# Performance work log

Hardware: AMD Instinct MI355X
Metric: run time of the kernel (lower is better)

The kernel has to match this reference:

```python
import jax, jax.numpy as jnp
import numpy as np
from jax import lax

N, C, H, W = 32, 128, 64, 64
EPS = 1e-5


def conv2d(x, w, stride=1, pad=0, dil=1, groups=1):
    return lax.conv_general_dilated(
        x, w, (stride, stride), [(pad, pad), (pad, pad)],
        rhs_dilation=(dil, dil), feature_group_count=groups,
        dimension_numbers=('NCHW', 'OIHW', 'NCHW'))


def bn(y):  # BatchNorm2d(affine=False), training-mode batch stats
    m = y.mean((0, 2, 3), keepdims=True)
    v = y.var((0, 2, 3), keepdims=True)
    return (y - m) * lax.rsqrt(v + EPS)


def max_pool3(x):
    return lax.reduce_window(x, -jnp.inf, lax.max, (1, 1, 3, 3), (1, 1, 1, 1),
                             [(0, 0), (0, 0), (1, 1), (1, 1)])


def avg_pool3(x):  # count_include_pad=False
    s = lax.reduce_window(x, 0., lax.add, (1, 1, 3, 3), (1, 1, 1, 1),
                          [(0, 0), (0, 0), (1, 1), (1, 1)])
    ones = jnp.ones((1, 1, x.shape[2], x.shape[3]), x.dtype)
    cnt = lax.reduce_window(ones, 0., lax.add, (1, 1, 3, 3), (1, 1, 1, 1),
                            [(0, 0), (0, 0), (1, 1), (1, 1)])
    return s / cnt


def setup_inputs() -> dict:
    key = jax.random.key(0)
    ks = jax.random.split(key, 20)
    sc = 0.05
    inp = {
        'x': jax.random.normal(ks[0], (N, C, H, W), jnp.float32),
        'weights': jax.random.uniform(ks[1], (8,), jnp.float32),
        'ca_fc1': jax.random.normal(ks[2], (C // 2, C, 1, 1), jnp.float32) * sc,
        'ca_fc2': jax.random.normal(ks[3], (C, C // 2, 1, 1), jnp.float32) * sc,
        'sa_conv': jax.random.normal(ks[4], (1, 2, 7, 7), jnp.float32) * sc,
        'sep3_dw1': jax.random.normal(ks[5], (C, 1, 3, 3), jnp.float32) * sc,
        'sep3_pw1': jax.random.normal(ks[6], (C, C, 1, 1), jnp.float32) * sc,
        'sep3_dw2': jax.random.normal(ks[7], (C, 1, 3, 3), jnp.float32) * sc,
        'sep3_pw2': jax.random.normal(ks[8], (C, C, 1, 1), jnp.float32) * sc,
        'sep5_dw1': jax.random.normal(ks[9], (C, 1, 5, 5), jnp.float32) * sc,
        'sep5_pw1': jax.random.normal(ks[10], (C, C, 1, 1), jnp.float32) * sc,
        'sep5_dw2': jax.random.normal(ks[11], (C, 1, 5, 5), jnp.float32) * sc,
        'sep5_pw2': jax.random.normal(ks[12], (C, C, 1, 1), jnp.float32) * sc,
        'dil3_dw': jax.random.normal(ks[13], (C, 1, 3, 3), jnp.float32) * sc,
        'dil3_pw': jax.random.normal(ks[14], (C, C, 1, 1), jnp.float32) * sc,
        'dil5_dw': jax.random.normal(ks[15], (C, 1, 5, 5), jnp.float32) * sc,
        'dil5_pw': jax.random.normal(ks[16], (C, C, 1, 1), jnp.float32) * sc,
        # stand-in for the random distinct bottom-quarter index selection
        'perm_idx': jax.random.permutation(ks[17], C // 4).astype(jnp.int32),
    }
    return inp


def _forward(x, weights, ca_fc1, ca_fc2, sa_conv,
             sep3_dw1, sep3_pw1, sep3_dw2, sep3_pw2,
             sep5_dw1, sep5_pw1, sep5_dw2, sep5_pw2,
             dil3_dw, dil3_pw, dil5_dw, dil5_pw, perm_idx):
    c = x.shape[1]
    # ---- spatial attention ----
    s = jnp.concatenate([x.mean(1, keepdims=True), x.max(1, keepdims=True)], 1)
    x = x * jax.nn.sigmoid(conv2d(s, sa_conv, pad=3))
    # ---- channel attention ----
    mlp = lambda z: conv2d(jax.nn.relu(conv2d(z, ca_fc1)), ca_fc2)
    att = jax.nn.sigmoid(mlp(x.mean((2, 3), keepdims=True)) +
                         mlp(x.max((2, 3), keepdims=True)))  # [N,C,1,1]
    x = x * att
    # ---- channel selection: top 3/4 by summed attention + permuted quarter ----
    slist = att.sum(0).reshape(c)
    _, top_idx = lax.top_k(slist, c * 3 // 4)
    num_dict = jnp.concatenate([top_idx.astype(jnp.int32), perm_idx])  # [C]
    xt = x[:, num_dict]
    # ---- 8 DARTS candidate ops, weighted sum ----
    def sep(y, dw1, pw1, dw2, pw2, pad):
        y = jax.nn.relu(y)
        y = bn(conv2d(conv2d(y, dw1, pad=pad, groups=c), pw1))
        y = jax.nn.relu(y)
        return bn(conv2d(conv2d(y, dw2, pad=pad, groups=c), pw2))

    def dil(y, dw, pw, pad):
        y = jax.nn.relu(y)
        return bn(conv2d(conv2d(y, dw, pad=pad, dil=2, groups=c), pw))

    temp1 = (weights[0] * jnp.zeros_like(xt)            # none
             + weights[1] * bn(max_pool3(xt))            # max_pool_3x3 + BN
             + weights[2] * bn(avg_pool3(xt))            # avg_pool_3x3 + BN
             + weights[3] * xt                           # skip_connect (stride=1)
             + weights[4] * sep(xt, sep3_dw1, sep3_pw1, sep3_dw2, sep3_pw2, 1)
             + weights[5] * sep(xt, sep5_dw1, sep5_pw1, sep5_dw2, sep5_pw2, 2)
             + weights[6] * dil(xt, dil3_dw, dil3_pw, 2)
             + weights[7] * dil(xt, dil5_dw, dil5_pw, 4))
    # scatter back (stride=1 => spatial sizes match)
    return x.at[:, num_dict].set(temp1)


def reference(x, weights, ca_fc1, ca_fc2, sa_conv,
              sep3_dw1, sep3_pw1, sep3_dw2, sep3_pw2,
              sep5_dw1, sep5_pw1, sep5_dw2, sep5_pw2,
              dil3_dw, dil3_pw, dil5_dw, dil5_pw, perm_idx):
    return _forward(x, weights, ca_fc1, ca_fc2, sa_conv,
                    sep3_dw1, sep3_pw1, sep3_dw2, sep3_pw2,
                    sep5_dw1, sep5_pw1, sep5_dw2, sep5_pw2,
                    dil3_dw, dil3_pw, dil5_dw, dil5_pw, perm_idx)
```

## Files before the change

kernel.cpp:

```cpp
#include <hip/hip_runtime.h>
#include <math.h>

#define DI __device__ __forceinline__
typedef unsigned short ush;

DI float u2f(ush u){ return __uint_as_float(((unsigned int)u)<<16); }
DI ush f2u(float f){ unsigned int u=__float_as_uint(f); u += 0x7fffu + ((u>>16)&1u); return (ush)(u>>16); }

constexpr int HWc = 4096;
constexpr float RCNT = 1.f/131072.f;
constexpr size_t BIG = 33554432ull;

typedef __attribute__((ext_vector_type(8))) __bf16 bf8;
typedef __attribute__((ext_vector_type(4))) float  f4;

DI void unp8(uint4 q, float* o){
  o[0]=u2f((ush)(q.x&0xffff)); o[1]=u2f((ush)(q.x>>16));
  o[2]=u2f((ush)(q.y&0xffff)); o[3]=u2f((ush)(q.y>>16));
  o[4]=u2f((ush)(q.z&0xffff)); o[5]=u2f((ush)(q.z>>16));
  o[6]=u2f((ush)(q.w&0xffff)); o[7]=u2f((ush)(q.w>>16));
}
DI uint4 pk8(const ush* u){
  uint4 q;
  q.x=(unsigned)u[0]|((unsigned)u[1]<<16); q.y=(unsigned)u[2]|((unsigned)u[3]<<16);
  q.z=(unsigned)u[4]|((unsigned)u[5]<<16); q.w=(unsigned)u[6]|((unsigned)u[7]<<16);
  return q;
}

__global__ void k_zero2(float* __restrict__ a, float* __restrict__ b){
  int i=blockIdx.x*256+threadIdx.x;
  if(i<2048) a[i]=0.f;
  else if(i<2048+49152) b[i-2048]=0.f;
}

__global__ void k_trivial(float* __restrict__ out){
  size_t i=(size_t)blockIdx.x*256+threadIdx.x;
  if(i<16777216ull) out[i]=0.f;
}

__global__ void k_chan_reduce(const float* __restrict__ x, float* __restrict__ smean, float* __restrict__ smax){
  int n = blockIdx.y;
  int px = blockIdx.x*256 + threadIdx.x;
  const float* xp = x + ((size_t)n*128)*HWc + px;
  float s=0.f, m=-INFINITY;
  #pragma unroll 8
  for(int c=0;c<128;c++){ float v=xp[(size_t)c*HWc]; s+=v; m=fmaxf(m,v); }
  smean[n*HWc+px]=s*(1.f/128.f);
  smax[n*HWc+px]=m;
}

__global__ void k_sa(const float* __restrict__ smean, const float* __restrict__ smax,
                     const float* __restrict__ w, float* __restrict__ sa){
  __shared__ float wm[49], wx[49];
  int t=threadIdx.x;
  if(t<49) wm[t]=w[t];
  else if(t<98) wx[t-49]=w[t];
  __syncthreads();
  int n=blockIdx.y;
  int px=blockIdx.x*256+t;
  int r=px>>6, c=px&63;
  const float* pm  = smean + n*HWc;
  const float* pxm = smax  + n*HWc;
  float acc=0.f;
  for(int ky=0;ky<7;ky++){
    int rr=r+ky-3; if(rr<0||rr>=64) continue;
    for(int kx=0;kx<7;kx++){
      int cc=c+kx-3; if(cc<0||cc>=64) continue;
      int q=(rr<<6)+cc;
      acc += wm[ky*7+kx]*pm[q] + wx[ky*7+kx]*pxm[q];
    }
  }
  sa[n*HWc+px] = 1.f/(1.f+expf(-acc));
}

__global__ void k_rowred(const float* __restrict__ x, const float* __restrict__ sa,
                         float* __restrict__ rsum, float* __restrict__ rmax){
  int c=blockIdx.x, n=blockIdx.y;
  const float* xp = x + ((size_t)n*128 + c)*HWc;
  const float* sp = sa + n*HWc;
  float s=0.f, m=-INFINITY;
  for(int i=threadIdx.x;i<HWc;i+=256){
    float v=xp[i]*sp[i]; s+=v; m=fmaxf(m,v);
  }
  __shared__ float ls[4], lm[4];
  for(int o=32;o>0;o>>=1){ s+=__shfl_down(s,o,64); m=fmaxf(m,__shfl_down(m,o,64)); }
  int lane=threadIdx.x&63, wv=threadIdx.x>>6;
  if(lane==0){ ls[wv]=s; lm[wv]=m; }
  __syncthreads();
  if(threadIdx.x==0){
    rsum[n*128+c]=ls[0]+ls[1]+ls[2]+ls[3];
    rmax[n*128+c]=fmaxf(fmaxf(lm[0],lm[1]),fmaxf(lm[2],lm[3]));
  }
}

__global__ void k_mlp(const float* __restrict__ rsum, const float* __restrict__ rmax,
                      const float* __restrict__ fc1, const float* __restrict__ fc2,
                      float* __restrict__ att){
  int n=blockIdx.x, t=threadIdx.x;
  __shared__ float zm[128], zx[128], hm[64], hx[64];
  if(t<128){ zm[t]=rsum[n*128+t]*(1.f/4096.f); zx[t]=rmax[n*128+t]; }
  __syncthreads();
  if(t<64){
    float a=0.f;
    for(int c=0;c<128;c++) a+=fc1[t*128+c]*zm[c];
    hm[t]=fmaxf(a,0.f);
  } else if(t<128){
    int j=t-64; float a=0.f;
    for(int c=0;c<128;c++) a+=fc1[j*128+c]*zx[c];
    hx[j]=fmaxf(a,0.f);
  }
  __syncthreads();
  if(t<128){
    float a=0.f,b=0.f;
    for(int j=0;j<64;j++){ float wv=fc2[t*64+j]; a+=wv*hm[j]; b+=wv*hx[j]; }
    att[n*128+t]=1.f/(1.f+expf(-(a+b)));
  }
}

__global__ void k_topk(const float* __restrict__ att, const int* __restrict__ perm,
                       int* __restrict__ nd_out, int* __restrict__ dst_pos){
  __shared__ float sl[128];
  __shared__ int nd[128];
  int t=threadIdx.x;
  float s=0.f;
  for(int n=0;n<32;n++) s+=att[n*128+t];
  sl[t]=s;
  nd[t]=t;
  __syncthreads();
  float v=sl[t]; int r=0;
  for(int c=0;c<128;c++){ float u=sl[c]; r += ((u>v) || (u==v && c<t)) ? 1 : 0; }
  if(r<96) nd[r]=t;
  __syncthreads();
  if(t<32) nd[96+t]=perm[t]&127;
  __syncthreads();
  nd_out[t]=nd[t]&127;
  int pos=-1;
  for(int p=0;p<128;p++) if((nd[p]&127)==t) pos=p;
  dst_pos[t]=pos;
}

template<int R,int S>
DI void stage_pads(float* __restrict__ Pl, int t){
  if(t<64){
    #pragma unroll
    for(int j=0;j<R;j++) Pl[t*S+j]=0.f;
    #pragma unroll
    for(int j=64+R;j<S;j++) Pl[t*S+j]=0.f;
  }
}

__global__ void k_cvt6(const float* __restrict__ a,const float* __restrict__ b,
    const float* __restrict__ c,const float* __restrict__ d,
    const float* __restrict__ e,const float* __restrict__ f,
    ush* __restrict__ wb){
  int z=blockIdx.y;
  const float* src = z==0?a:z==1?b:z==2?c:z==3?d:z==4?e:f;
  int i=blockIdx.x*256+threadIdx.x;
  wb[z*16384+i]=f2u(src[i]);
}

__global__ __launch_bounds__(256) void k_xtps(const float* __restrict__ x,
    const float* __restrict__ sa, const float* __restrict__ att,
    const int* __restrict__ nd, ush* __restrict__ bufX, float* __restrict__ stats){
  constexpr int S=68;
  __shared__ float Pl[64*S];
  int p=blockIdx.x, n=blockIdx.y, t=threadIdx.x;
  int ch=nd[p]&127;
  float a=att[n*128+ch];
  const float* xp=x+((size_t)n*128+ch)*HWc;
  const float* sp=sa+n*HWc;
  int px0=t*16;
  ush u[16];
  #pragma unroll
  for(int j=0;j<4;j++){
    float4 xv=*(const float4*)(xp+px0+4*j);
    float4 sv=*(const float4*)(sp+px0+4*j);
    u[4*j+0]=f2u(xv.x*sv.x*a); u[4*j+1]=f2u(xv.y*sv.y*a);
    u[4*j+2]=f2u(xv.z*sv.z*a); u[4*j+3]=f2u(xv.w*sv.w*a);
  }
  ush* bo=bufX+((size_t)n*128+p)*HWc+px0;
  *(uint4*)bo   = pk8(u);
  *(uint4*)(bo+8)= pk8(u+8);
  float* dst=&Pl[(px0>>6)*S + 1 + (px0&63)];
  #pragma unroll
  for(int i=0;i<16;i++) dst[i]=u2f(u[i]);
  stage_pads<1,S>(Pl,t);
  __syncthreads();
  int r=t>>2, c0=(t&3)*16;
  float s[16], m[16];
  #pragma unroll
  for(int i=0;i<16;i++){ s[i]=0.f; m[i]=-INFINITY; }
  int rin=0;
  #pragma unroll
  for(int ky=-1;ky<=1;ky++){
    int rr=r+ky;
    if(rr<0||rr>=64) continue;
    rin++;
    float row[20];
    #pragma unroll
    for(int j=0;j<5;j++) *(float4*)&row[4*j] = *(const float4*)&Pl[rr*S + c0 + 4*j];
    float e0  = (c0==0)  ? -INFINITY : row[0];
    float e17 = (c0==48) ? -INFINITY : row[17];
    #pragma unroll
    for(int i=0;i<16;i++){
      float lf = (i==0)  ? e0  : row[i];
      float rg = (i==15) ? e17 : row[i+2];
      s[i] += row[i]+row[i+1]+row[i+2];
      m[i] = fmaxf(m[i], fmaxf(lf, fmaxf(row[i+1], rg)));
    }
  }
  float sm=0,qm=0,sv=0,qv=0;
  #pragma unroll
  for(int i=0;i<16;i++){
    int c=c0+i;
    float cnt=(float)(rin*(3-(c==0)-(c==63)));
    float ap=s[i]/cnt, mp=m[i];
    sm+=mp; qm+=mp*mp; sv+=ap; qv+=ap*ap;
  }
  for(int o=32;o>0;o>>=1){
    sm+=__shfl_down(sm,o,64); qm+=__shfl_down(qm,o,64);
    sv+=__shfl_down(sv,o,64); qv+=__shfl_down(qv,o,64);
  }
  __shared__ float l[4][4];
  int lane=t&63, wv=t>>6;
  if(lane==0){ l[wv][0]=sm; l[wv][1]=qm; l[wv][2]=sv; l[wv][3]=qv; }
  __syncthreads();
  if(t==0){
    atomicAdd(&stats[p],     l[0][0]+l[1][0]+l[2][0]+l[3][0]);
    atomicAdd(&stats[128+p], l[0][1]+l[1][1]+l[2][1]+l[3][1]);
    atomicAdd(&stats[256+p], l[0][2]+l[1][2]+l[2][2]+l[3][2]);
    atomicAdd(&stats[384+p], l[0][3]+l[1][3]+l[2][3]+l[3][3]);
  }
}

template<int KS,int DIL,int BN>
DI void dw_core(float* Pl, const ush* src, const float* __restrict__ dww,
                const float* __restrict__ fin, int p,int n,int t, ush* outb){
  constexpr int R=(KS/2)*DIL;
  constexpr int S=(R==4)?76:68;
  constexpr int NL=(16+2*R+3)/4;
  float mean=0.f, rstd=0.f;
  if constexpr(BN){ mean=fin[p]; rstd=fin[128+p]; }
  const ush* bp = src + ((size_t)n*128+p)*HWc;
  int px0=t*16;
  uint4 va=*(const uint4*)(bp+px0);
  uint4 vb=*(const uint4*)(bp+px0+8);
  float* dst=&Pl[(px0>>6)*S + R + (px0&63)];
  unsigned int wv8[8]={va.x,va.y,va.z,va.w,vb.x,vb.y,vb.z,vb.w};
  #pragma unroll
  for(int j=0;j<8;j++){
    float v0=u2f((ush)(wv8[j]&0xffff)), v1=u2f((ush)(wv8[j]>>16));
    if constexpr(BN){ v0=(v0-mean)*rstd; v1=(v1-mean)*rstd; }
    dst[2*j]  =fmaxf(v0,0.f);
    dst[2*j+1]=fmaxf(v1,0.f);
  }
  stage_pads<R,S>(Pl,t);
  __syncthreads();
  float wk[KS*KS];
  #pragma unroll
  for(int i=0;i<KS*KS;i++) wk[i]=dww[p*KS*KS+i];
  int r=t>>2, c0=(t&3)*16;
  float acc[16];
  #pragma unroll
  for(int i=0;i<16;i++) acc[i]=0.f;
  #pragma unroll
  for(int ky=0;ky<KS;ky++){
    int rr=r+(ky-KS/2)*DIL;
    if(rr<0||rr>=64) continue;
    float row[NL*4];
    #pragma unroll
    for(int j=0;j<NL;j++) *(float4*)&row[4*j] = *(const float4*)&Pl[rr*S + c0 + 4*j];
    #pragma unroll
    for(int kx=0;kx<KS;kx++){
      float wv=wk[ky*KS+kx];
      #pragma unroll
      for(int i=0;i<16;i++) acc[i]+=wv*row[R + i + (kx-KS/2)*DIL];
    }
  }
  ush* op = outb + ((size_t)n*128+p)*HWc + r*64 + c0;
  #pragma unroll
  for(int q=0;q<4;q++){
    ushort4 vv;
    vv.x=f2u(acc[4*q+0]); vv.y=f2u(acc[4*q+1]);
    vv.z=f2u(acc[4*q+2]); vv.w=f2u(acc[4*q+3]);
    *(ushort4*)(op+4*q)=vv;
  }
}

__global__ __launch_bounds__(256) void k_dw4(const ush* __restrict__ bufX,
    const float* __restrict__ s3d1,const float* __restrict__ s5d1,
    const float* __restrict__ d3dw,const float* __restrict__ d5dw,
    ush* __restrict__ bufA, ush* __restrict__ bufB,
    ush* __restrict__ bufC, ush* __restrict__ bufD){
  __shared__ float Pl[64*76];
  int p=blockIdx.x,n=blockIdx.y,t=threadIdx.x,z=blockIdx.z;
  if(z==0)      dw_core<3,1,0>(Pl,bufX,s3d1,nullptr,p,n,t,bufA);
  else if(z==1) dw_core<5,1,0>(Pl,bufX,s5d1,nullptr,p,n,t,bufB);
  else if(z==2) dw_core<3,2,0>(Pl,bufX,d3dw,nullptr,p,n,t,bufC);
  else          dw_core<5,2,0>(Pl,bufX,d5dw,nullptr,p,n,t,bufD);
}

__global__ __launch_bounds__(256) void k_dw2(ush* bufA, ush* bufB,
    const float* __restrict__ s3d2,const float* __restrict__ s5d2,
    const float* __restrict__ fin0,const float* __restrict__ fin2){
  __shared__ float Pl[64*68];
  int p=blockIdx.x,n=blockIdx.y,t=threadIdx.x,z=blockIdx.z;
  if(z==0) dw_core<3,1,1>(Pl,bufA,s3d2,fin0,p,n,t,bufA);
  else     dw_core<5,1,1>(Pl,bufB,s5d2,fin2,p,n,t,bufB);
}

DI void pw_core(char* pool, const ush* dwin, const ush* __restrict__ wt,
                ush* outb, float* __restrict__ shad, int bx,int by,int t){
  ush (*Bt)[132] = (ush(*)[132])pool;
  float* Lf = (float*)pool;
  int n=by;
  int px0b = bx*64;
  const ush* dp = dwin + ((size_t)n*128)*HWc + px0b;
  #pragma unroll
  for(int k=0;k<4;k++){
    int e = t + k*256;
    int c2 = e>>4;
    int p4 = (e&15)*4;
    const ush* g0 = dp + (size_t)(2*c2)*HWc + p4;
    ushort4 va = *(const ushort4*)g0;
    ushort4 vb = *(const ushort4*)(g0 + HWc);
    *(unsigned int*)&Bt[p4+0][2*c2] = (unsigned int)va.x | ((unsigned int)vb.x<<16);
    *(unsigned int*)&Bt[p4+1][2*c2] = (unsigned int)va.y | ((unsigned int)vb.y<<16);
    *(unsigned int*)&Bt[p4+2][2*c2] = (unsigned int)va.z | ((unsigned int)vb.z<<16);
    *(unsigned int*)&Bt[p4+3][2*c2] = (unsigned int)va.w | ((unsigned int)vb.w<<16);
  }
  int lane=t&63, wv=t>>6;
  int co0=(wv>>1)*64, pxw=(wv&1)*32;
  int g=lane>>4, sl=lane&15;
  int arow = co0 + sl;
  int acg  = g*8;
  bf8 a[4][4];
  #pragma unroll
  for(int mt=0;mt<4;mt++)
    #pragma unroll
    for(int kt=0;kt<4;kt++)
      a[mt][kt] = *(const bf8*)(wt + (size_t)(arow+mt*16)*128 + kt*32 + acg);
  f4 acc[4][2] = {};
  __syncthreads();
  #pragma unroll
  for(int nt=0;nt<2;nt++){
    int pxl = pxw + nt*16 + sl;
    bf8 b[4];
    #pragma unroll
    for(int kt=0;kt<4;kt++){
      union { uint2 h[2]; bf8 v; } u;
      const ush* bp = &Bt[pxl][kt*32 + acg];
      u.h[0] = *(const uint2*)bp;
      u.h[1] = *(const uint2*)(bp+4);
      b[kt] = u.v;
    }
    #pragma unroll
    for(int kt=0;kt<4;kt++)
      #pragma unroll
      for(int mt=0;mt<4;mt++)
        acc[mt][nt] = __builtin_amdgcn_mfma_f32_16x16x32_bf16(a[mt][kt], b[kt], acc[mt][nt], 0,0,0);
  }
  __syncthreads();
  #pragma unroll
  for(int mt=0;mt<4;mt++)
    #pragma unroll
    for(int r=0;r<4;r++){
      int co = co0 + mt*16 + g*4 + r;
      Lf[co*66 + pxw + sl]      = acc[mt][0][r];
      Lf[co*66 + pxw + 16 + sl] = acc[mt][1][r];
    }
  __syncthreads();
  int co=t>>1, half=t&1;
  const float* Lr = &Lf[co*66 + half*32];
  float s1=0.f, s2=0.f;
  ush ob16[32];
  #pragma unroll
  for(int j=0;j<16;j++){
    float2 v=*(const float2*)(Lr+2*j);
    s1+=v.x+v.y; s2+=v.x*v.x+v.y*v.y;
    ob16[2*j]=f2u(v.x); ob16[2*j+1]=f2u(v.y);
  }
  s1+=__shfl_xor(s1,1,64); s2+=__shfl_xor(s2,1,64);
  ush* op = outb + ((size_t)n*128+co)*HWc + px0b + half*32;
  *(uint4*)op      = pk8(ob16);
  *(uint4*)(op+8)  = pk8(ob16+8);
  *(uint4*)(op+16) = pk8(ob16+16);
  *(uint4*)(op+24) = pk8(ob16+24);
  float* sh = shad + (((bx + by)&31)*256);
  if(half==0){ atomicAdd(&sh[co],s1); atomicAdd(&sh[128+co],s2); }
}

__global__ __launch_bounds__(256) void k_pw4(ush* bA, ush* bB, ush* bC, ush* bD,
    const ush* __restrict__ w0,const ush* __restrict__ w1,
    const ush* __restrict__ w2,const ush* __restrict__ w3,
    float* __restrict__ s0,float* __restrict__ s1,
    float* __restrict__ s2,float* __restrict__ s3){
  __shared__ __align__(16) char pool[33792];
  int z=blockIdx.z;
  ush* b = z==0?bA:z==1?bB:z==2?bC:bD;
  const ush* wt = z==0?w0:z==1?w1:z==2?w2:w3;
  float* sh = z==0?s0:z==1?s1:z==2?s2:s3;
  pw_core(pool,b,wt,b,sh,blockIdx.x,blockIdx.y,threadIdx.x);
}

__global__ void k_statfin4(const float* __restrict__ s0,const float* __restrict__ s1,
    const float* __restrict__ s2,const float* __restrict__ s3,
    float* __restrict__ f0,float* __restrict__ f1,
    float* __restrict__ f2,float* __restrict__ f3){
  int z=blockIdx.x, t=threadIdx.x;
  const float* shd = z==0?s0:z==1?s1:z==2?s2:s3;
  float* fin = z==0?f0:z==1?f1:z==2?f2:f3;
  if(t<128){
    float su=0.f, sq=0.f;
    #pragma unroll
    for(int j=0;j<32;j++){ su+=shd[j*256+t]; sq+=shd[j*256+128+t]; }
    float mean=su*RCNT, var=sq*RCNT-mean*mean;
    fin[t]=mean;
    fin[128+t]=rsqrtf(var+1e-5f);
  }
}

__global__ __launch_bounds__(256) void k_bacc(const float* __restrict__ x,
    const float* __restrict__ sa, const float* __restrict__ att,
    const int* __restrict__ nd, const int* __restrict__ dpos,
    const float* __restrict__ stats,
    const float* __restrict__ fin1,const float* __restrict__ fin3,
    const float* __restrict__ fin4,const float* __restrict__ fin5,
    const float* __restrict__ wts, const ush* __restrict__ bufX,
    const ush* __restrict__ brA,const ush* __restrict__ brB,
    const ush* __restrict__ brC,const ush* __restrict__ brD,
    float* __restrict__ out){
  constexpr int S=68;
  __shared__ float Pl[64*S];
  int ch=blockIdx.x, n=blockIdx.y, t=threadIdx.x;
  int p=dpos[ch];
  if(p<0){
    float a=att[n*128+ch];
    const float* xp=x+((size_t)n*128+ch)*HWc;
    const float* sp=sa+n*HWc;
    float* op=out+((size_t)n*128+ch)*HWc;
    int px0=t*16;
    #pragma unroll
    for(int j=0;j<4;j++){
      float4 xv=*(const float4*)(xp+px0+4*j);
      float4 sv=*(const float4*)(sp+px0+4*j);
      float4 ov;
      ov.x=xv.x*sv.x*a; ov.y=xv.y*sv.y*a; ov.z=xv.z*sv.z*a; ov.w=xv.w*sv.w*a;
      *(float4*)(op+px0+4*j)=ov;
    }
    return;
  }
  const ush* bxp=bufX+((size_t)n*128+p)*HWc;
  int px0=t*16;
  uint4 qa=*(const uint4*)(bxp+px0), qb=*(const uint4*)(bxp+px0+8);
  {
    float tv[16];
    unp8(qa,tv); unp8(qb,tv+8);
    float* dst=&Pl[(px0>>6)*S + 1 + (px0&63)];
    #pragma unroll
    for(int i=0;i<16;i++) dst[i]=tv[i];
  }
  stage_pads<1,S>(Pl,t);
  __syncthreads();
  float w1=wts[1],w2=wts[2],w3=wts[3],w4=wts[4],w5=wts[5],w6=wts[6],w7=wts[7];
  float m0,r0v,m1,r1v;
  { float su=stats[p],     sq=stats[128+p]; float mean=su*RCNT,var=sq*RCNT-mean*mean; m0=mean; r0v=rsqrtf(var+1e-5f); }
  { float su=stats[256+p], sq=stats[384+p]; float mean=su*RCNT,var=sq*RCNT-mean*mean; m1=mean; r1v=rsqrtf(var+1e-5f); }
  float mA=fin1[p],rA=fin1[128+p], mB=fin3[p],rB=fin3[128+p];
  float mC=fin4[p],rC=fin4[128+p], mD=fin5[p],rD=fin5[128+p];
  int r=t>>2, c0=(t&3)*16;
  float s[16], m[16], crow[16];
  #pragma unroll
  for(int i=0;i<16;i++){ s[i]=0.f; m[i]=-INFINITY; }
  int rin=0;
  #pragma unroll
  for(int ky=-1;ky<=1;ky++){
    int rr=r+ky;
    if(rr<0||rr>=64) continue;
    rin++;
    float row[20];
    #pragma unroll
    for(int j=0;j<5;j++) *(float4*)&row[4*j] = *(const float4*)&Pl[rr*S + c0 + 4*j];
    if(ky==0){
      #pragma unroll
      for(int i=0;i<16;i++) crow[i]=row[i+1];
    }
    float e0  = (c0==0)  ? -INFINITY : row[0];
    float e17 = (c0==48) ? -INFINITY : row[17];
    #pragma unroll
    for(int i=0;i<16;i++){
      float lf = (i==0)  ? e0  : row[i];
      float rg = (i==15) ? e17 : row[i+2];
      s[i] += row[i]+row[i+1]+row[i+2];
      m[i] = fmaxf(m[i], fmaxf(lf, fmaxf(row[i+1], rg)));
    }
  }
  float vout[16];
  #pragma unroll
  for(int i=0;i<16;i++){
    int c=c0+i;
    float cnt=(float)(rin*(3-(c==0)-(c==63)));
    float ap=s[i]/cnt;
    vout[i] = w3*crow[i] + w1*(m[i]-m0)*r0v + w2*(ap-m1)*r1v;
  }
  size_t boff=((size_t)n*128+p)*HWc + r*64 + c0;
  {
    float tv[16];
    unp8(*(const uint4*)(brA+boff),tv); unp8(*(const uint4*)(brA+boff+8),tv+8);
    #pragma unroll
    for(int i=0;i<16;i++) vout[i]+=w4*(tv[i]-mA)*rA;
    unp8(*(const uint4*)(brB+boff),tv); unp8(*(const uint4*)(brB+boff+8),tv+8);
    #pragma unroll
    for(int i=0;i<16;i++) vout[i]+=w5*(tv[i]-mB)*rB;
    unp8(*(const uint4*)(brC+boff),tv); unp8(*(const uint4*)(brC+boff+8),tv+8);
    #pragma unroll
    for(int i=0;i<16;i++) vout[i]+=w6*(tv[i]-mC)*rC;
    unp8(*(const uint4*)(brD+boff),tv); unp8(*(const uint4*)(brD+boff+8),tv+8);
    #pragma unroll
    for(int i=0;i<16;i++) vout[i]+=w7*(tv[i]-mD)*rD;
  }
  float* op=out+((size_t)n*128+ch)*HWc + r*64 + c0;
  #pragma unroll
  for(int q=0;q<4;q++) *(float4*)(op+4*q)=*(float4*)&vout[4*q];
}

extern "C" void kernel_launch(void* const* d_in, const int* in_sizes, int n_in,
                              void* d_out, int out_size, void* d_ws, size_t ws_size,
                              hipStream_t stream){
  (void)in_sizes; (void)n_in; (void)out_size;
  const float* x   =(const float*)d_in[0];
  const float* wts =(const float*)d_in[1];
  const float* fc1 =(const float*)d_in[2];
  const float* fc2 =(const float*)d_in[3];
  const float* saw =(const float*)d_in[4];
  const float* s3d1=(const float*)d_in[5];
  const float* s3p1=(const float*)d_in[6];
  const float* s3d2=(const float*)d_in[7];
  const float* s3p2=(const float*)d_in[8];
  const float* s5d1=(const float*)d_in[9];
  const float* s5p1=(const float*)d_in[10];
  const float* s5d2=(const float*)d_in[11];
  const float* s5p2=(const float*)d_in[12];
  const float* d3dw=(const float*)d_in[13];
  const float* d3pw=(const float*)d_in[14];
  const float* d5dw=(const float*)d_in[15];
  const float* d5pw=(const float*)d_in[16];
  const int* perm=(const int*)d_in[17];
  float* out=(float*)d_out;

  char* w=(char*)d_ws;
  float* stats=(float*)w;  w+=8192;
  float* smean=(float*)w;  w+=524288;
  float* smax =(float*)w;  w+=524288;
  float* sa   =(float*)w;  w+=524288;
  float* rsum =(float*)w;  w+=16384;
  float* rmax =(float*)w;  w+=16384;
  float* att  =(float*)w;  w+=16384;
  int*   nd   =(int*)w;    w+=512;
  int*   dpos =(int*)w;    w+=512;
  size_t small_bytes=(size_t)(w-(char*)d_ws);
  ush* bufA=(ush*)w;
  ush* bufB=(ush*)(w+BIG);
  ush* bufC=(ush*)(w+2*BIG);
  ush* bufD=(ush*)(w+3*BIG);
  ush* bufX=(ush*)(w+4*BIG);

  if(ws_size < small_bytes + 5*BIG){
    k_trivial<<<dim3(65536),dim3(256),0,stream>>>(out);
    return;
  }

  ush* wb=(ush*)smean;
  ush* wb_s3p1=wb;
  ush* wb_s3p2=wb+16384;
  ush* wb_s5p1=wb+32768;
  ush* wb_s5p2=wb+49152;
  ush* wb_d3pw=wb+65536;
  ush* wb_d5pw=wb+81920;

  float* shd0=smax;
  float* shd1=smax+ 8192;
  float* shd2=smax+16384;
  float* shd3=smax+24576;
  float* shd4=smax+32768;
  float* shd5=smax+40960;

  float* fin0=stats+ 512;
  float* fin1=stats+ 768;
  float* fin2=stats+1024;
  float* fin3=stats+1280;
  float* fin4=stats+1536;
  float* fin5=stats+1792;

  dim3 B(256);
  dim3 Gpn(128,32);
  k_chan_reduce<<<dim3(16,32),B,0,stream>>>(x,smean,smax);
  k_sa<<<dim3(16,32),B,0,stream>>>(smean,smax,saw,sa);
  k_zero2<<<dim3(200),B,0,stream>>>(stats,smax);
  k_cvt6<<<dim3(64,6),B,0,stream>>>(s3p1,s3p2,s5p1,s5p2,d3pw,d5pw,wb);
  k_rowred<<<dim3(128,32),B,0,stream>>>(x,sa,rsum,rmax);
  k_mlp<<<dim3(32),B,0,stream>>>(rsum,rmax,fc1,fc2,att);
  k_topk<<<dim3(1),dim3(128),0,stream>>>(att,perm,nd,dpos);
  k_xtps<<<Gpn,B,0,stream>>>(x,sa,att,nd,bufX,stats);
  k_dw4<<<dim3(128,32,4),B,0,stream>>>(bufX,s3d1,s5d1,d3dw,d5dw,bufA,bufB,bufC,bufD);
  k_pw4<<<dim3(64,32,4),B,0,stream>>>(bufA,bufB,bufC,bufD,
      wb_s3p1,wb_s5p1,wb_d3pw,wb_d5pw, shd0,shd2,shd4,shd5);
  k_statfin4<<<dim3(4),dim3(128),0,stream>>>(shd0,shd2,shd4,shd5,fin0,fin2,fin4,fin5);
  k_dw2<<<dim3(128,32,2),B,0,stream>>>(bufA,bufB,s3d2,s5d2,fin0,fin2);
  k_pw4<<<dim3(64,32,2),B,0,stream>>>(bufA,bufB,bufA,bufA,
      wb_s3p2,wb_s5p2,wb_s3p2,wb_s3p2, shd1,shd3,shd1,shd1);
  k_statfin4<<<dim3(2),dim3(128),0,stream>>>(shd1,shd3,shd1,shd1,fin1,fin3,fin1,fin1);
  k_bacc<<<Gpn,B,0,stream>>>(x,sa,att,nd,dpos,stats,fin1,fin3,fin4,fin5,
      wts,bufX,bufA,bufB,bufC,bufD,out);
}
```

Baseline: 470.5 us.

## Enlarge pointwise-conv tiles and loop each block over several pixel chunks

The pointwise MFMA conv kernel now makes each block loop over four 128-pixel chunks, instead of handling one 64-pixel tile. Each wave computes a 64x64 output sub-tile, and the write-back is split into two channel halves so the larger tile fits in the same shared-memory pool. The grid shrinks eightfold and the BN-stat atomics shrink accordingly. The aim is to cut per-block overhead and atomic traffic. In exchange there are fewer blocks to hide latency, the chunk loop has no overlap of loads with compute, and weight fragments are re-read from global memory on every chunk.

```diff
diff --git a/kernel.cpp b/kernel.cpp
--- a/kernel.cpp
+++ b/kernel.cpp
@@ -314,83 +314,89 @@
   ush (*Bt)[132] = (ush(*)[132])pool;
   float* Lf = (float*)pool;
   int n=by;
-  int px0b = bx*64;
-  const ush* dp = dwin + ((size_t)n*128)*HWc + px0b;
-  #pragma unroll
-  for(int k=0;k<4;k++){
-    int e = t + k*256;
-    int c2 = e>>4;
-    int p4 = (e&15)*4;
-    const ush* g0 = dp + (size_t)(2*c2)*HWc + p4;
-    ushort4 va = *(const ushort4*)g0;
-    ushort4 vb = *(const ushort4*)(g0 + HWc);
-    *(unsigned int*)&Bt[p4+0][2*c2] = (unsigned int)va.x | ((unsigned int)vb.x<<16);
-    *(unsigned int*)&Bt[p4+1][2*c2] = (unsigned int)va.y | ((unsigned int)vb.y<<16);
-    *(unsigned int*)&Bt[p4+2][2*c2] = (unsigned int)va.z | ((unsigned int)vb.z<<16);
-    *(unsigned int*)&Bt[p4+3][2*c2] = (unsigned int)va.w | ((unsigned int)vb.w<<16);
-  }
   int lane=t&63, wv=t>>6;
-  int co0=(wv>>1)*64, pxw=(wv&1)*32;
+  int co0=(wv>>1)*64, pxh=(wv&1)*64;
   int g=lane>>4, sl=lane&15;
-  int arow = co0 + sl;
-  int acg  = g*8;
-  bf8 a[4][4];
-  #pragma unroll
-  for(int mt=0;mt<4;mt++)
-    #pragma unroll
-    for(int kt=0;kt<4;kt++)
-      a[mt][kt] = *(const bf8*)(wt + (size_t)(arow+mt*16)*128 + kt*32 + acg);
-  f4 acc[4][2] = {};
-  __syncthreads();
-  #pragma unroll
-  for(int nt=0;nt<2;nt++){
-    int pxl = pxw + nt*16 + sl;
-    bf8 b[4];
+  int acg = g*8;
+  float* sh = shad + (((bx + by)&31)*256);
+
+  for(int w=0;w<4;w++){
+    int px0 = (bx*4 + w)*128;
+    const ush* dp = dwin + ((size_t)n*128)*HWc + px0;
+    #pragma unroll
+    for(int k=0;k<8;k++){
+      int e = t + k*256;
+      int c2 = e>>5;
+      int p4 = (e&31)*4;
+      const ush* g0 = dp + (size_t)(2*c2)*HWc + p4;
+      ushort4 va = *(const ushort4*)g0;
+      ushort4 vb = *(const ushort4*)(g0 + HWc);
+      *(unsigned int*)&Bt[p4+0][2*c2] = (unsigned int)va.x | ((unsigned int)vb.x<<16);
+      *(unsigned int*)&Bt[p4+1][2*c2] = (unsigned int)va.y | ((unsigned int)vb.y<<16);
+      *(unsigned int*)&Bt[p4+2][2*c2] = (unsigned int)va.z | ((unsigned int)vb.z<<16);
+      *(unsigned int*)&Bt[p4+3][2*c2] = (unsigned int)va.w | ((unsigned int)vb.w<<16);
+    }
+    __syncthreads();
+    f4 acc[4][4] = {};
     #pragma unroll
     for(int kt=0;kt<4;kt++){
-      union { uint2 h[2]; bf8 v; } u;
-      const ush* bp = &Bt[pxl][kt*32 + acg];
-      u.h[0] = *(const uint2*)bp;
-      u.h[1] = *(const uint2*)(bp+4);
-      b[kt] = u.v;
-    }
-    #pragma unroll
-    for(int kt=0;kt<4;kt++)
+      bf8 ak[4];
       #pragma unroll
       for(int mt=0;mt<4;mt++)
-        acc[mt][nt] = __builtin_amdgcn_mfma_f32_16x16x32_bf16(a[mt][kt], b[kt], acc[mt][nt], 0,0,0);
-  }
-  __syncthreads();
-  #pragma unroll
-  for(int mt=0;mt<4;mt++)
-    #pragma unroll
-    for(int r=0;r<4;r++){
-      int co = co0 + mt*16 + g*4 + r;
-      Lf[co*66 + pxw + sl]      = acc[mt][0][r];
-      Lf[co*66 + pxw + 16 + sl] = acc[mt][1][r];
-    }
-  __syncthreads();
-  int co=t>>1, half=t&1;
-  const float* Lr = &Lf[co*66 + half*32];
-  float s1=0.f, s2=0.f;
-  ush ob16[32];
-  #pragma unroll
-  for(int j=0;j<16;j++){
-    float2 v=*(const float2*)(Lr+2*j);
-    s1+=v.x+v.y; s2+=v.x*v.x+v.y*v.y;
-    ob16[2*j]=f2u(v.x); ob16[2*j+1]=f2u(v.y);
-  }
-  s1+=__shfl_xor(s1,1,64); s2+=__shfl_xor(s2,1,64);
-  ush* op = outb + ((size_t)n*128+co)*HWc + px0b + half*32;
-  *(uint4*)op      = pk8(ob16);
-  *(uint4*)(op+8)  = pk8(ob16+8);
-  *(uint4*)(op+16) = pk8(ob16+16);
-  *(uint4*)(op+24) = pk8(ob16+24);
-  float* sh = shad + (((bx + by)&31)*256);
-  if(half==0){ atomicAdd(&sh[co],s1); atomicAdd(&sh[128+co],s2); }
-}
-
-__global__ __launch_bounds__(256) void k_pw4(ush* bA, ush* bB, ush* bC, ush* bD,
+        ak[mt] = *(const bf8*)(wt + (size_t)(co0+mt*16+sl)*128 + kt*32 + acg);
+      #pragma unroll
+      for(int nt=0;nt<4;nt++){
+        union { uint2 h[2]; bf8 v; } u;
+        const ush* bp = &Bt[pxh + nt*16 + sl][kt*32 + acg];
+        u.h[0] = *(const uint2*)bp;
+        u.h[1] = *(const uint2*)(bp+4);
+        #pragma unroll
+        for(int mt=0;mt<4;mt++)
+          acc[mt][nt] = __builtin_amdgcn_mfma_f32_16x16x32_bf16(ak[mt], u.v, acc[mt][nt], 0,0,0);
+      }
+    }
+    __syncthreads();
+    #pragma unroll
+    for(int h=0;h<2;h++){
+      if((wv>>1)==h){
+        #pragma unroll
+        for(int mt=0;mt<4;mt++)
+          #pragma unroll
+          for(int r=0;r<4;r++){
+            int lco = mt*16 + g*4 + r;
+            #pragma unroll
+            for(int nt=0;nt<4;nt++)
+              Lf[lco*130 + pxh + nt*16 + sl] = acc[mt][nt][r];
+          }
+      }
+      __syncthreads();
+      {
+        int lco=t>>2, q=t&3;
+        const float* Lr = &Lf[lco*130 + q*32];
+        float s1=0.f, s2=0.f;
+        ush ob16[32];
+        #pragma unroll
+        for(int j=0;j<16;j++){
+          float2 v=*(const float2*)(Lr+2*j);
+          s1+=v.x+v.y; s2+=v.x*v.x+v.y*v.y;
+          ob16[2*j]=f2u(v.x); ob16[2*j+1]=f2u(v.y);
+        }
+        s1+=__shfl_xor(s1,1,64); s2+=__shfl_xor(s2,1,64);
+        s1+=__shfl_xor(s1,2,64); s2+=__shfl_xor(s2,2,64);
+        int co = h*64 + lco;
+        ush* op = outb + ((size_t)n*128+co)*HWc + px0 + q*32;
+        *(uint4*)op      = pk8(ob16);
+        *(uint4*)(op+8)  = pk8(ob16+8);
+        *(uint4*)(op+16) = pk8(ob16+16);
+        *(uint4*)(op+24) = pk8(ob16+24);
+        if(q==0){ atomicAdd(&sh[co],s1); atomicAdd(&sh[128+co],s2); }
+      }
+      __syncthreads();
+    }
+  }
+}
+
+__global__ __launch_bounds__(256) void k_pwm(ush* bA, ush* bB, ush* bC, ush* bD,
     const ush* __restrict__ w0,const ush* __restrict__ w1,
     const ush* __restrict__ w2,const ush* __restrict__ w3,
     float* __restrict__ s0,float* __restrict__ s1,
@@ -603,11 +609,11 @@
   k_topk<<<dim3(1),dim3(128),0,stream>>>(att,perm,nd,dpos);
   k_xtps<<<Gpn,B,0,stream>>>(x,sa,att,nd,bufX,stats);
   k_dw4<<<dim3(128,32,4),B,0,stream>>>(bufX,s3d1,s5d1,d3dw,d5dw,bufA,bufB,bufC,bufD);
-  k_pw4<<<dim3(64,32,4),B,0,stream>>>(bufA,bufB,bufC,bufD,
+  k_pwm<<<dim3(8,32,4),B,0,stream>>>(bufA,bufB,bufC,bufD,
       wb_s3p1,wb_s5p1,wb_d3pw,wb_d5pw, shd0,shd2,shd4,shd5);
   k_statfin4<<<dim3(4),dim3(128),0,stream>>>(shd0,shd2,shd4,shd5,fin0,fin2,fin4,fin5);
   k_dw2<<<dim3(128,32,2),B,0,stream>>>(bufA,bufB,s3d2,s5d2,fin0,fin2);
-  k_pw4<<<dim3(64,32,2),B,0,stream>>>(bufA,bufB,bufA,bufA,
+  k_pwm<<<dim3(8,32,2),B,0,stream>>>(bufA,bufB,bufA,bufA,
       wb_s3p2,wb_s5p2,wb_s3p2,wb_s3p2, shd1,shd3,shd1,shd1);
   k_statfin4<<<dim3(2),dim3(128),0,stream>>>(shd1,shd3,shd1,shd1,fin1,fin3,fin1,fin1);
   k_bacc<<<Gpn,B,0,stream>>>(x,sa,att,nd,dpos,stats,fin1,fin3,fin4,fin5,
```

Result: faster. 459.4 us (-2.4%).
